# Optimization experiments

Measured on AMD Instinct MI355X. Metric: run time of the kernel, lower is better.

Reference implementation:

```python
import jax, jax.numpy as jnp
import numpy as np


def setup_inputs() -> dict:
    key = jax.random.key(0)
    k1, k2 = jax.random.split(key)
    B, C, F, H, W = 2, 19, 4, 256, 384
    inp = jax.random.uniform(k1, (B, C, F, H, W), dtype=jnp.float32)
    target = jax.random.randint(k2, (B, F, H, W), 0, C, dtype=jnp.int64)
    return {"input": inp, "target": target}


def reference(input, target):
    """Multi-class Lovasz-Softmax loss, vectorized over classes.

    input:  [B, C, F, H, W] class probabilities in [0, 1]
    target: [B, F, H, W] integer labels in [0, C)
    (No ignore_index values present in the generated inputs, so the
    valid-pixel filter of the original is a no-op.)
    """
    B, C, F, H, W = input.shape
    # flatten to [N, C] pixels-by-classes, matching permute(0,2,3,4,1).view(-1,C)
    probs = jnp.transpose(input, (0, 2, 3, 4, 1)).reshape(-1, C)
    labels = target.reshape(-1)  # [N]

    fg = (labels[:, None] == jnp.arange(C)[None, :]).astype(probs.dtype)  # [N, C]
    errors = jnp.abs(fg - probs)  # [N, C]

    # descending sort per class column (one batched sort instead of C kernels)
    perm = jnp.argsort(-errors, axis=0)  # [N, C]
    errors_sorted = jnp.take_along_axis(errors, perm, axis=0)
    fg_sorted = jnp.take_along_axis(fg, perm, axis=0)

    # Lovasz gradient (Alg. 1), per class
    gts = jnp.sum(fg, axis=0)  # [C]
    intersection = gts[None, :] - jnp.cumsum(fg_sorted, axis=0)
    union = gts[None, :] + jnp.cumsum(1.0 - fg_sorted, axis=0)
    jaccard = 1.0 - intersection / union
    grad = jnp.concatenate([jaccard[:1], jaccard[1:] - jaccard[:-1]], axis=0)

    per_class_loss = jnp.sum(errors_sorted * grad, axis=0)  # [C]

    # mean over classes that are present (fg.sum() > 0), like the loop's `continue`
    present = gts > 0
    n_present = jnp.maximum(jnp.sum(present.astype(probs.dtype)), 1.0)
    return jnp.sum(jnp.where(present, per_class_loss, 0.0)) / n_present
```

## Files before the change

kernel.cpp:

```cpp
#include <hip/hip_runtime.h>


#define NCLS   19
#define FHW    393216
#define NPIX   786432
#define NB     1024
#define PIXPB  8192
#define NCHUNK (NPIX / PIXPB)
#define BPT    (NB / 256)

#define GH_WORDS  (NCLS * NB)
#define TOT_WORDS (GH_WORDS + 4)

__device__ __forceinline__ void accum_one(unsigned int* h, float p, int lab, int c) {
    const bool fg = (lab == c);
    const float e = fg ? (1.0f - p) : p;
    unsigned int bits = __float_as_uint(1.0f + e);
    unsigned int bkt = (bits - 0x3F800000u) >> 13;
    bkt = min(bkt, (unsigned int)(NB - 1));
    atomicAdd(&h[bkt], 1u + ((unsigned int)fg << 20));
}

__global__ __launch_bounds__(256) void zero_kernel(unsigned int* __restrict__ ws) {
    const int i = blockIdx.x * 256 + threadIdx.x;
    if (i < TOT_WORDS) ws[i] = 0u;
}

__global__ __launch_bounds__(256) void hist_kernel(
        const float* __restrict__ input, const int* __restrict__ target,
        unsigned int* __restrict__ gH) {
    __shared__ unsigned int h[NB];
    const int tid = threadIdx.x;
    const int c = blockIdx.x;
    const int chunk = blockIdx.y;

    #pragma unroll
    for (int i = tid; i < NB; i += 256) h[i] = 0u;
    __syncthreads();

    const int pix0 = chunk * PIXPB;
    const int b = pix0 / FHW;
    const int fhw0 = pix0 % FHW;
    const float4* __restrict__ p4 =
        (const float4*)(input + ((long long)(b * NCLS + c)) * FHW + fhw0);
    const int4* __restrict__ l4 = (const int4*)(target + pix0);

    #pragma unroll
    for (int i = tid; i < PIXPB / 4; i += 256) {
        float4 p = p4[i];
        int4 l = l4[i];
        accum_one(h, p.x, l.x, c);
        accum_one(h, p.y, l.y, c);
        accum_one(h, p.z, l.z, c);
        accum_one(h, p.w, l.w, c);
    }
    __syncthreads();

    unsigned long long* __restrict__ g64 =
        (unsigned long long*)(gH + c * NB);
    #pragma unroll
    for (int i = tid; i < NB / 2; i += 256) {
        const unsigned long long v =
            (unsigned long long)h[2 * i] |
            ((unsigned long long)h[2 * i + 1] << 32);
        if (v) atomicAdd(&g64[i], v);
    }
}

__global__ __launch_bounds__(256) void scan_kernel(
        const unsigned int* __restrict__ gH, unsigned int* __restrict__ acc,
        float* __restrict__ out) {
    const int c = blockIdx.x;
    const int tid = threadIdx.x;
    const unsigned int* __restrict__ g = gH + c * NB;

    unsigned int w[BPT];
    const int base = NB - BPT * (tid + 1);
    unsigned int sumN = 0, sumG = 0;
    #pragma unroll
    for (int j = 0; j < BPT; ++j) {
        w[j] = g[base + j];
        sumN += w[j] & 0xFFFFFu;
        sumG += w[j] >> 20;
    }

    __shared__ unsigned long long sd[256];
    const unsigned long long mine = ((unsigned long long)sumG << 32) | sumN;
    sd[tid] = mine;
    __syncthreads();
    for (int off = 1; off < 256; off <<= 1) {
        unsigned long long add = (tid >= off) ? sd[tid - off] : 0ull;
        __syncthreads();
        sd[tid] += add;
        __syncthreads();
    }
    const unsigned long long incl = sd[tid];
    const unsigned long long tot = sd[255];
    const unsigned long long exc = incl - mine;
    const unsigned int G = (unsigned int)(tot >> 32);

    float accv = 0.0f;
    if (G != 0u) {
        const float Gf = (float)G;
        unsigned int r = (unsigned int)exc;
        unsigned int cf = (unsigned int)(exc >> 32);
        float Jprev = __fdividef((float)r, Gf + (float)r - (float)cf);
        #pragma unroll
        for (int j = BPT - 1; j >= 0; --j) {
            const unsigned int nb = w[j] & 0xFFFFFu;
            const unsigned int gb = w[j] >> 20;
            r += nb; cf += gb;
            if (nb) {
                const float Jnew = __fdividef((float)r, Gf + (float)r - (float)cf);
                const float center = ((float)(base + j) + 0.5f) * (1.0f / (float)NB);
                accv += center * (Jnew - Jprev);
                Jprev = Jnew;
            }
        }
    }

    __shared__ float sf[256];
    sf[tid] = accv;
    __syncthreads();
    for (int off = 128; off > 0; off >>= 1) {
        if (tid < off) sf[tid] += sf[tid + off];
        __syncthreads();
    }
    if (tid == 0) {
        if (G != 0u) {
            atomicAdd((float*)&acc[0], sf[0]);
            atomicAdd(&acc[1], 1u);
        }
        __threadfence();
        const unsigned int t = atomicAdd(&acc[2], 1u);
        if (t == NCLS - 1) {
            const float s = atomicAdd((float*)&acc[0], 0.0f);
            const unsigned int k = atomicAdd(&acc[1], 0u);
            out[0] = s / fmaxf((float)k, 1.0f);
        }
    }
}

extern "C" void kernel_launch(void* const* d_in, const int* in_sizes, int n_in,
                              void* d_out, int out_size, void* d_ws, size_t ws_size,
                              hipStream_t stream) {
    const float* input = (const float*)d_in[0];
    const int* target = (const int*)d_in[1];
    float* out = (float*)d_out;

    unsigned int* ws = (unsigned int*)d_ws;
    unsigned int* gH = ws;
    unsigned int* acc = gH + GH_WORDS;

    zero_kernel<<<(TOT_WORDS + 255) / 256, 256, 0, stream>>>(ws);
    hist_kernel<<<dim3(NCLS, NCHUNK), 256, 0, stream>>>(input, target, gH);
    scan_kernel<<<NCLS, 256, 0, stream>>>(gH, acc, out);
}
```

Baseline: 101.4 us.

## Fuse histogram and scan kernels using per-class last-block ticket

Merges the scan kernel into the histogram kernel. Each block takes a per-class ticket counter after flushing its histogram atomics, and the last block for each class performs the scan and loss accumulation. This removes one kernel launch and the inter-kernel gap. In exchange, every block pays for a ticket atomic and a barrier, and correctness now depends on memory ordering via s_waitcnt and atomic loads rather than a full threadfence.

```diff
diff --git a/kernel.cpp b/kernel.cpp
--- a/kernel.cpp
+++ b/kernel.cpp
@@ -10,7 +10,7 @@
 #define BPT    (NB / 256)
 
 #define GH_WORDS  (NCLS * NB)
-#define TOT_WORDS (GH_WORDS + 4)
+#define TOT_WORDS (GH_WORDS + NCLS + 4)
 
 __device__ __forceinline__ void accum_one(unsigned int* h, float p, int lab, int c) {
     const bool fg = (lab == c);
@@ -26,13 +26,15 @@
     if (i < TOT_WORDS) ws[i] = 0u;
 }
 
-__global__ __launch_bounds__(256) void hist_kernel(
+__global__ __launch_bounds__(256) void fused_kernel(
         const float* __restrict__ input, const int* __restrict__ target,
-        unsigned int* __restrict__ gH) {
+        unsigned int* __restrict__ gH, float* __restrict__ out) {
     __shared__ unsigned int h[NB];
     const int tid = threadIdx.x;
     const int c = blockIdx.x;
     const int chunk = blockIdx.y;
+    unsigned int* __restrict__ tick = gH + GH_WORDS;
+    unsigned int* __restrict__ acc  = tick + NCLS;
 
     #pragma unroll
     for (int i = tid; i < NB; i += 256) h[i] = 0u;
@@ -56,8 +58,8 @@
     }
     __syncthreads();
 
-    unsigned long long* __restrict__ g64 =
-        (unsigned long long*)(gH + c * NB);
+    unsigned int* __restrict__ g = gH + c * NB;
+    unsigned long long* __restrict__ g64 = (unsigned long long*)g;
     #pragma unroll
     for (int i = tid; i < NB / 2; i += 256) {
         const unsigned long long v =
@@ -65,21 +67,23 @@
             ((unsigned long long)h[2 * i + 1] << 32);
         if (v) atomicAdd(&g64[i], v);
     }
-}
+    __syncthreads();
 
-__global__ __launch_bounds__(256) void scan_kernel(
-        const unsigned int* __restrict__ gH, unsigned int* __restrict__ acc,
-        float* __restrict__ out) {
-    const int c = blockIdx.x;
-    const int tid = threadIdx.x;
-    const unsigned int* __restrict__ g = gH + c * NB;
+    __shared__ unsigned int sdone;
+    if (tid == 0) {
+        asm volatile("s_waitcnt vmcnt(0)" ::: "memory");
+        sdone = atomicAdd(&tick[c], 1u);
+    }
+    __syncthreads();
+    if (sdone != NCHUNK - 1) return;
 
     unsigned int w[BPT];
     const int base = NB - BPT * (tid + 1);
     unsigned int sumN = 0, sumG = 0;
     #pragma unroll
     for (int j = 0; j < BPT; ++j) {
-        w[j] = g[base + j];
+        w[j] = __hip_atomic_load(&g[base + j], __ATOMIC_RELAXED,
+                                 __HIP_MEMORY_SCOPE_AGENT);
         sumN += w[j] & 0xFFFFFu;
         sumG += w[j] >> 20;
     }
@@ -131,7 +135,7 @@
             atomicAdd((float*)&acc[0], sf[0]);
             atomicAdd(&acc[1], 1u);
         }
-        __threadfence();
+        asm volatile("s_waitcnt vmcnt(0)" ::: "memory");
         const unsigned int t = atomicAdd(&acc[2], 1u);
         if (t == NCLS - 1) {
             const float s = atomicAdd((float*)&acc[0], 0.0f);
@@ -149,10 +153,7 @@
     float* out = (float*)d_out;
 
     unsigned int* ws = (unsigned int*)d_ws;
-    unsigned int* gH = ws;
-    unsigned int* acc = gH + GH_WORDS;
 
     zero_kernel<<<(TOT_WORDS + 255) / 256, 256, 0, stream>>>(ws);
-    hist_kernel<<<dim3(NCLS, NCHUNK), 256, 0, stream>>>(input, target, gH);
-    scan_kernel<<<NCLS, 256, 0, stream>>>(gH, acc, out);
+    fused_kernel<<<dim3(NCLS, NCHUNK), 256, 0, stream>>>(input, target, ws, out);
 }
```

After: 112.9 us. 11.3% more time.
